# Kernel tuning notes

Measured on AMD Instinct MI355X. Metric: run time of the kernel, lower is better.

The kernel has to match this reference:

```python
import jax, jax.numpy as jnp
import numpy as np

SIZE = 2048
N_TASKS = 8
REDUCTION = 16
HID = SIZE // REDUCTION  # 128
B = 4096
INIT_STD = 0.01


def setup_inputs() -> dict:
    key = jax.random.key(0)
    k1, k2, k3 = jax.random.split(key, 3)
    x = jax.random.normal(k1, (B, SIZE), dtype=jnp.float32)
    task_id = jax.random.randint(k2, (B,), 0, N_TASKS, dtype=jnp.int64)
    kd, ku = jax.random.split(k3)
    # torch Linear weight is [out, in]; store transposed [in, out] per task
    Wd = jax.random.normal(kd, (N_TASKS, SIZE, HID), dtype=jnp.float32) * INIT_STD
    bd = jnp.zeros((N_TASKS, HID), dtype=jnp.float32)
    Wu = jax.random.normal(ku, (N_TASKS, HID, SIZE), dtype=jnp.float32) * INIT_STD
    bu = jnp.zeros((N_TASKS, SIZE), dtype=jnp.float32)
    return {"x": x, "Wd": Wd, "bd": bd, "Wu": Wu, "bu": bu, "task_id": task_id}


def reference(x, Wd, bd, Wu, bu, task_id):
    # residual=True (default). Compute every expert's adapter output densely
    # (T small), then combine per-sample by task_id; task_id == -1 -> passthrough.
    h = jax.nn.silu(jnp.einsum('bd,tdh->bth', x, Wd) + bd[None])        # [B,T,HID]
    out_all = jnp.einsum('bth,thd->btd', h, Wu) + bu[None]              # [B,T,SIZE]
    tid = jnp.clip(task_id, 0, N_TASKS - 1)
    out_sel = jnp.take_along_axis(out_all, tid[:, None, None], axis=1)[:, 0]  # [B,SIZE]
    valid = (task_id >= 0)[:, None]
    return jnp.where(valid, x + out_sel, x)
```

## Files before the change

### kernel.cpp

```cpp
#include <hip/hip_runtime.h>

#define BN 4096
#define SZ 2048
#define HIDN 128
#define NT 8
#define PADROWS 4384
#define PADTILES (PADROWS / 16)

typedef __bf16 bf16_t;
typedef bf16_t bf16x4 __attribute__((ext_vector_type(4)));
typedef bf16_t bf16x8 __attribute__((ext_vector_type(8)));
typedef float f32x4 __attribute__((ext_vector_type(4)));

__device__ inline bf16_t f2b(float f) {
    unsigned u = __builtin_bit_cast(unsigned, f);
    unsigned short s = (unsigned short)((u + 0x7fffu + ((u >> 16) & 1u)) >> 16);
    return __builtin_bit_cast(bf16_t, s);
}


__device__ inline int detect_i64(const int* task, int tid, int* sflag) {
    if (tid < 64) {
        int v = task[2 * tid + 1];
        bool ok = (v == 0 || v == -1);
        unsigned long long m = __ballot(ok);
        if (tid == 0) *sflag = (m == ~0ull) ? 1 : 0;
    }
    return 0;
}

__global__ __launch_bounds__(256) void k_prep(const float* __restrict__ Wd,
                                              const int* __restrict__ task,
                                              bf16_t* __restrict__ WdP,
                                              int* __restrict__ cnt16g) {
    int bid = blockIdx.x, tid = threadIdx.x;
    __shared__ int wv[4][9], sflag;
    if (bid >= 512) {
        int blk = bid - 512;
        int lane = tid & 63, w = tid >> 6;
        detect_i64(task, tid, &sflag);
        __syncthreads();
        int f = sflag;
        int item = blk * 256 + tid;
        int tv = f ? task[2 * item] : task[item];
        int bk = (tv < 0) ? 8 : (tv > 7 ? 7 : tv);
#pragma unroll
        for (int bu = 0; bu < 9; bu++) {
            unsigned long long m = __ballot(bk == bu);
            if (lane == 0) wv[w][bu] = (int)__popcll(m);
        }
        __syncthreads();
        if (tid < 9) {
            int s = 0;
#pragma unroll
            for (int ww = 0; ww < 4; ww++) s += wv[ww][tid];
            cnt16g[blk * 9 + tid] = s;
        }
        return;
    }
    __shared__ float tile[32][132];
    int t = bid >> 6, kt = bid & 63;
    const float* src = Wd + ((size_t)t * SZ + kt * 32) * HIDN;
    bf16_t* dst = WdP + ((size_t)(t * 8) * 64 + kt) * 512;
#pragma unroll
    for (int i = 0; i < 4; i++) {
        int row = (tid >> 5) + 8 * i, quad = tid & 31;
        f32x4 v = *(const f32x4*)(src + (size_t)row * HIDN + quad * 4);
        tile[row][quad * 4 + 0] = v.x; tile[row][quad * 4 + 1] = v.y;
        tile[row][quad * 4 + 2] = v.z; tile[row][quad * 4 + 3] = v.w;
    }
    __syncthreads();
    int w = tid >> 6, lane = tid & 63, lr = lane & 15, lq = lane >> 4;
#pragma unroll
    for (int ii = 0; ii < 2; ii++) {
        int hf = w * 2 + ii;
        bf16x8 o;
#pragma unroll
        for (int j = 0; j < 8; j++) {
            int kloc = (j < 4) ? (4 * lq + j) : (16 + 4 * lq + j - 4);
            o[j] = f2b(tile[kloc][hf * 16 + lr]);
        }
        *(bf16x8*)(dst + (size_t)hf * 64 * 512 + lane * 8) = o;
    }
}

__global__ __launch_bounds__(256) void k_scatter(const int* __restrict__ task,
                                                 const int* __restrict__ cnt16g,
                                                 int* __restrict__ meta,
                                                 int* __restrict__ idxb) {
    __shared__ int c16s[16][9], tot[9], pre9[9], off[10], wv[4][9], sflag;
    int tid = threadIdx.x, lane = tid & 63, w = tid >> 6, blk = blockIdx.x;
    detect_i64(task, tid, &sflag);
    if (tid < 144) ((int*)c16s)[tid] = cnt16g[tid];
    __syncthreads();
    int f = sflag;
    int item = blk * 256 + tid;
    int tv = f ? task[2 * item] : task[item];
    int bk = (tv < 0) ? 8 : (tv > 7 ? 7 : tv);
    unsigned long long mymask = 0;
#pragma unroll
    for (int bu = 0; bu < 9; bu++) {
        unsigned long long m = __ballot(bk == bu);
        if (lane == 0) wv[w][bu] = (int)__popcll(m);
        if (bk == bu) mymask = m;
    }
    int rank = (int)__popcll(mymask & ((1ull << lane) - 1ull));
    __syncthreads();
    if (tid < 9) {
        int t = 0;
#pragma unroll
        for (int b = 0; b < 16; b++) t += c16s[b][tid];
        tot[tid] = t;
        int p = 0;
        for (int b = 0; b < blk; b++) p += c16s[b][tid];
        pre9[tid] = p;
        int s = 0;
#pragma unroll
        for (int ww = 0; ww < 4; ww++) { int q = wv[ww][tid]; wv[ww][tid] = s; s += q; }
    }
    __syncthreads();
    if (tid == 0) {
        int s = 0;
        for (int i = 0; i < 9; i++) { off[i] = s; s += (tot[i] + 31) & ~31; }
        off[9] = s;
    }
    __syncthreads();
    int pos = off[bk] + pre9[bk] + wv[w][bk] + rank;
    idxb[pos] = item;
    if (blk == 0) {
        if (tid < 9) meta[tid] = tot[tid];
        if (tid >= 16 && tid < 26) meta[tid] = off[tid - 16];
    }
}

__global__ __launch_bounds__(256) void k_gemm1(const float* __restrict__ x,
                                               const float* __restrict__ Wu,
                                               const bf16_t* __restrict__ WdP,
                                               bf16_t* __restrict__ WuP,
                                               const float* __restrict__ bd,
                                               const int* __restrict__ idxb,
                                               const int* __restrict__ meta,
                                               bf16_t* __restrict__ HbP) {
    int bid = blockIdx.x;
    int tid = threadIdx.x, lane = tid & 63, w = tid >> 6;
    int lr = lane & 15, lq = lane >> 4;
    if (bid >= 4096) {
        __shared__ float tile[32][132];
        int lb = bid - 4096;
        int t = lb >> 6, rem = lb & 63;
        int kf = rem >> 4, cch = rem & 15;
        const float* src = Wu + ((size_t)t * HIDN + kf * 32) * SZ + cch * 128;
        bf16_t* dst = WuP + ((size_t)(t * 128 + cch * 8) * 4 + kf) * 512;
#pragma unroll
        for (int i = 0; i < 4; i++) {
            int row = (tid >> 5) + 8 * i, quad = tid & 31;
            f32x4 v = *(const f32x4*)(src + (size_t)row * SZ + quad * 4);
            tile[row][quad * 4 + 0] = v.x; tile[row][quad * 4 + 1] = v.y;
            tile[row][quad * 4 + 2] = v.z; tile[row][quad * 4 + 3] = v.w;
        }
        __syncthreads();
#pragma unroll
        for (int ii = 0; ii < 2; ii++) {
            int hf = w * 2 + ii;
            bf16x8 o;
#pragma unroll
            for (int j = 0; j < 8; j++) {
                int kloc = (j < 4) ? (4 * lq + j) : (16 + 4 * lq + j - 4);
                o[j] = f2b(tile[kloc][hf * 16 + lr]);
            }
            *(bf16x8*)(dst + (size_t)hf * 4 * 512 + lane * 8) = o;
        }
        return;
    }
    int t = bid & 7, hh = (bid >> 3) & 1, tile = bid >> 4;
    int n = meta[t];
    int r0 = tile * 16;
    if (r0 >= n) return;
    int base = meta[16 + t];

    __shared__ int sg[16];
    __shared__ bf16_t xl[2][16][260];
    __shared__ bf16_t hl[16][68];
    if (tid < 16) {
        int r = r0 + tid;
        sg[tid] = idxb[base + (r < n ? r : n - 1)];
    }
    __syncthreads();

    f32x4 pre[4];
#pragma unroll
    for (int rr = 0; rr < 4; rr++)
        pre[rr] = *(const f32x4*)(x + (size_t)sg[w * 4 + rr] * SZ + lane * 4);
#pragma unroll
    for (int rr = 0; rr < 4; rr++) {
        bf16x4 v = {f2b(pre[rr].x), f2b(pre[rr].y), f2b(pre[rr].z), f2b(pre[rr].w)};
        *(bf16x4*)(&xl[0][w * 4 + rr][lane * 4]) = v;
    }
    __syncthreads();

    const bf16_t* wb = WdP + ((size_t)(t * 8 + hh * 4 + w) * 64) * 512 + lane * 8;
    f32x4 acc = {};
    for (int c = 0; c < 8; c++) {
        int cur = c & 1;
        if (c < 7) {
#pragma unroll
            for (int rr = 0; rr < 4; rr++)
                pre[rr] = *(const f32x4*)(x + (size_t)sg[w * 4 + rr] * SZ +
                                          (c + 1) * 256 + lane * 4);
        }
#pragma unroll
        for (int k8 = 0; k8 < 8; k8++) {
            int kf = c * 8 + k8;
            bf16x4 alo = *(const bf16x4*)(&xl[cur][lr][k8 * 32 + 4 * lq]);
            bf16x4 ahi = *(const bf16x4*)(&xl[cur][lr][k8 * 32 + 16 + 4 * lq]);
            bf16x8 a;
            a[0] = alo[0]; a[1] = alo[1]; a[2] = alo[2]; a[3] = alo[3];
            a[4] = ahi[0]; a[5] = ahi[1]; a[6] = ahi[2]; a[7] = ahi[3];
            bf16x8 b = *(const bf16x8*)(wb + (size_t)kf * 512);
            acc = __builtin_amdgcn_mfma_f32_16x16x32_bf16(a, b, acc, 0, 0, 0);
        }
        if (c < 7) {
#pragma unroll
            for (int rr = 0; rr < 4; rr++) {
                bf16x4 v = {f2b(pre[rr].x), f2b(pre[rr].y), f2b(pre[rr].z), f2b(pre[rr].w)};
                *(bf16x4*)(&xl[cur ^ 1][w * 4 + rr][lane * 4]) = v;
            }
        }
        __syncthreads();
    }

    {
        float bb = bd[t * HIDN + hh * 64 + w * 16 + lr];
#pragma unroll
        for (int reg = 0; reg < 4; reg++) {
            float v = acc[reg] + bb;
            hl[4 * lq + reg][w * 16 + lr] = f2b(v / (1.f + __expf(-v)));
        }
    }
    __syncthreads();
    if (w < 2) {
        int rt = (base + r0) >> 4;
        bf16x8 o;
#pragma unroll
        for (int j = 0; j < 8; j++) {
            int k = w * 32 + ((j < 4) ? (4 * lq + j) : (16 + 4 * lq + j - 4));
            o[j] = hl[lr][k];
        }
        *(bf16x8*)(HbP + ((size_t)(rt * 4 + hh * 2 + w) * 64 + lane) * 8) = o;
    }
}

__global__ __launch_bounds__(256) void k_gemm2(const float* __restrict__ x,
                                               const bf16_t* __restrict__ WuP,
                                               const float* __restrict__ bu,
                                               const bf16_t* __restrict__ HbP,
                                               const int* __restrict__ idxb,
                                               const int* __restrict__ meta,
                                               float* __restrict__ out) {
    int bid = blockIdx.x;
    int tid = threadIdx.x;
    if (bid >= 16384) {
        int pb = bid - 16384;
        int n8 = meta[8];
        int tile = pb & 127, half = pb >> 7;
        int r0 = tile * 32;
        if (r0 >= n8) return;
        int base8 = meta[16 + 8];
        int row = tid >> 3, cq = tid & 7;
        int r = r0 + row;
        if (r < n8) {
            int g = idxb[base8 + r];
            const f32x4* xs = (const f32x4*)(x + (size_t)g * SZ + half * 256) + cq;
            f32x4* os = (f32x4*)(out + (size_t)g * SZ + half * 256) + cq;
#pragma unroll
            for (int j = 0; j < 8; j++) __builtin_nontemporal_store(xs[j * 8], &os[j * 8]);
        }
        return;
    }
    int t = bid & 7, tile = (bid >> 3) & 127, cchunk = bid >> 10;
    int n = meta[t];
    int r0 = tile * 32;
    if (r0 >= n) return;
    int base = meta[16 + t];
    int lane = tid & 63, w = tid >> 6;
    int wr = w & 1, wc = w >> 1, lr = lane & 15, lq = lane >> 4;

    int rt = (base + r0) / 16 + wr;
    const bf16_t* ap = HbP + (size_t)rt * 4 * 512 + lane * 8;
    bf16x8 a[4];
#pragma unroll
    for (int kf = 0; kf < 4; kf++) a[kf] = *(const bf16x8*)(ap + kf * 512);

    const bf16_t* bp = WuP + ((size_t)(t * 128 + cchunk * 8 + wc * 4) * 4) * 512 + lane * 8;
    f32x4 acc[4] = {};
#pragma unroll
    for (int cf = 0; cf < 4; cf++) {
#pragma unroll
        for (int kf = 0; kf < 4; kf++) {
            bf16x8 b = *(const bf16x8*)(bp + (size_t)(cf * 4 + kf) * 512);
            acc[cf] = __builtin_amdgcn_mfma_f32_16x16x32_bf16(a[kf], b, acc[cf], 0, 0, 0);
        }
    }

    int gr[4];
#pragma unroll
    for (int reg = 0; reg < 4; reg++) {
        int r = r0 + wr * 16 + 4 * lq + reg;
        gr[reg] = (r < n) ? idxb[base + r] : -1;
    }
#pragma unroll
    for (int cf = 0; cf < 4; cf++) {
        int c = cchunk * 128 + wc * 64 + cf * 16 + lr;
        float bb = bu[t * SZ + c];
#pragma unroll
        for (int reg = 0; reg < 4; reg++) {
            if (gr[reg] >= 0) {
                size_t o = (size_t)gr[reg] * SZ + c;
                __builtin_nontemporal_store(x[o] + acc[cf][reg] + bb, &out[o]);
            }
        }
    }
}

extern "C" void kernel_launch(void* const* d_in, const int* in_sizes, int n_in,
                              void* d_out, int out_size, void* d_ws, size_t ws_size,
                              hipStream_t stream) {
    const float* x  = (const float*)d_in[0];
    const float* Wd = (const float*)d_in[1];
    const float* bd = (const float*)d_in[2];
    const float* Wu = (const float*)d_in[3];
    const float* bu = (const float*)d_in[4];
    const int* task = (const int*)d_in[5];
    float* out = (float*)d_out;

    char* ws = (char*)d_ws;
    int* idxb    = (int*)ws;
    int* meta    = (int*)(ws + 17664);
    int* cnt16   = (int*)(ws + 17920);
    bf16_t* HbP  = (bf16_t*)(ws + 18560);
    bf16_t* WdP  = (bf16_t*)(ws + 1140864);
    bf16_t* WuP  = (bf16_t*)(ws + 5335168);

    k_prep<<<528, 256, 0, stream>>>(Wd, task, WdP, cnt16);
    k_scatter<<<16, 256, 0, stream>>>(task, cnt16, meta, idxb);
    k_gemm1<<<4096 + 512, 256, 0, stream>>>(x, Wu, WdP, WuP, bd, idxb, meta, HbP);
    k_gemm2<<<16384 + 1024, 256, 0, stream>>>(x, WuP, bu, HbP, idxb, meta, out);
}
```

Baseline: 48.73 us.

## Merge scatter into prep kernel and split MFMA accumulator chain

Drops the separate k_scatter launch. Each of the 16 bucketing blocks in k_prep now redundantly scans all 4096 task ids to compute the global per-bucket counts and prefix offsets itself, then writes its own items into idxb. This removes one kernel launch and the global count round-trip, at the cost of 16x redundant counting work and many block barriers. Separately, the gemm1 inner loop alternates between two accumulators so consecutive MFMAs are not serially dependent, and sums them at the end.

```diff
diff --git a/kernel.cpp b/kernel.cpp
--- a/kernel.cpp
+++ b/kernel.cpp
@@ -19,42 +19,66 @@
 }
 
 
-__device__ inline int detect_i64(const int* task, int tid, int* sflag) {
-    if (tid < 64) {
-        int v = task[2 * tid + 1];
-        bool ok = (v == 0 || v == -1);
-        unsigned long long m = __ballot(ok);
-        if (tid == 0) *sflag = (m == ~0ull) ? 1 : 0;
-    }
-    return 0;
-}
-
 __global__ __launch_bounds__(256) void k_prep(const float* __restrict__ Wd,
                                               const int* __restrict__ task,
                                               bf16_t* __restrict__ WdP,
-                                              int* __restrict__ cnt16g) {
+                                              int* __restrict__ meta,
+                                              int* __restrict__ idxb) {
     int bid = blockIdx.x, tid = threadIdx.x;
-    __shared__ int wv[4][9], sflag;
     if (bid >= 512) {
+        __shared__ int c16s[16][9], tot[9], pre9[9], off[10], wv[4][9], sflag;
         int blk = bid - 512;
         int lane = tid & 63, w = tid >> 6;
-        detect_i64(task, tid, &sflag);
+        if (tid < 64) {
+            int v = task[2 * tid + 1];
+            bool ok = (v == 0 || v == -1);
+            unsigned long long m = __ballot(ok);
+            if (tid == 0) sflag = (m == ~0ull) ? 1 : 0;
+        }
         __syncthreads();
         int f = sflag;
-        int item = blk * 256 + tid;
-        int tv = f ? task[2 * item] : task[item];
-        int bk = (tv < 0) ? 8 : (tv > 7 ? 7 : tv);
-#pragma unroll
-        for (int bu = 0; bu < 9; bu++) {
-            unsigned long long m = __ballot(bk == bu);
-            if (lane == 0) wv[w][bu] = (int)__popcll(m);
-        }
-        __syncthreads();
+        int mybk = 0, myrank = 0, myprew = 0;
+        for (int s = 0; s < 16; s++) {
+            int item = s * 256 + tid;
+            int tv = f ? task[2 * item] : task[item];
+            int bk = (tv < 0) ? 8 : (tv > 7 ? 7 : tv);
+            unsigned long long mymask = 0;
+#pragma unroll
+            for (int bu = 0; bu < 9; bu++) {
+                unsigned long long m = __ballot(bk == bu);
+                if (lane == 0) wv[w][bu] = (int)__popcll(m);
+                if (bk == bu) mymask = m;
+            }
+            __syncthreads();
+            if (s == blk) {
+                mybk = bk;
+                myrank = (int)__popcll(mymask & ((1ull << lane) - 1ull));
+                myprew = 0;
+                for (int ww = 0; ww < w; ww++) myprew += wv[ww][bk];
+            }
+            if (tid < 9) c16s[s][tid] = wv[0][tid] + wv[1][tid] + wv[2][tid] + wv[3][tid];
+            __syncthreads();
+        }
         if (tid < 9) {
+            int t = 0;
+#pragma unroll
+            for (int s = 0; s < 16; s++) t += c16s[s][tid];
+            tot[tid] = t;
+            int p = 0;
+            for (int s = 0; s < blk; s++) p += c16s[s][tid];
+            pre9[tid] = p;
+        }
+        __syncthreads();
+        if (tid == 0) {
             int s = 0;
-#pragma unroll
-            for (int ww = 0; ww < 4; ww++) s += wv[ww][tid];
-            cnt16g[blk * 9 + tid] = s;
+            for (int i = 0; i < 9; i++) { off[i] = s; s += (tot[i] + 31) & ~31; }
+            off[9] = s;
+        }
+        __syncthreads();
+        idxb[off[mybk] + pre9[mybk] + myprew + myrank] = blk * 256 + tid;
+        if (blk == 0) {
+            if (tid < 9) meta[tid] = tot[tid];
+            if (tid >= 16 && tid < 26) meta[tid] = off[tid - 16];
         }
         return;
     }
@@ -81,55 +105,6 @@
             o[j] = f2b(tile[kloc][hf * 16 + lr]);
         }
         *(bf16x8*)(dst + (size_t)hf * 64 * 512 + lane * 8) = o;
-    }
-}
-
-__global__ __launch_bounds__(256) void k_scatter(const int* __restrict__ task,
-                                                 const int* __restrict__ cnt16g,
-                                                 int* __restrict__ meta,
-                                                 int* __restrict__ idxb) {
-    __shared__ int c16s[16][9], tot[9], pre9[9], off[10], wv[4][9], sflag;
-    int tid = threadIdx.x, lane = tid & 63, w = tid >> 6, blk = blockIdx.x;
-    detect_i64(task, tid, &sflag);
-    if (tid < 144) ((int*)c16s)[tid] = cnt16g[tid];
-    __syncthreads();
-    int f = sflag;
-    int item = blk * 256 + tid;
-    int tv = f ? task[2 * item] : task[item];
-    int bk = (tv < 0) ? 8 : (tv > 7 ? 7 : tv);
-    unsigned long long mymask = 0;
-#pragma unroll
-    for (int bu = 0; bu < 9; bu++) {
-        unsigned long long m = __ballot(bk == bu);
-        if (lane == 0) wv[w][bu] = (int)__popcll(m);
-        if (bk == bu) mymask = m;
-    }
-    int rank = (int)__popcll(mymask & ((1ull << lane) - 1ull));
-    __syncthreads();
-    if (tid < 9) {
-        int t = 0;
-#pragma unroll
-        for (int b = 0; b < 16; b++) t += c16s[b][tid];
-        tot[tid] = t;
-        int p = 0;
-        for (int b = 0; b < blk; b++) p += c16s[b][tid];
-        pre9[tid] = p;
-        int s = 0;
-#pragma unroll
-        for (int ww = 0; ww < 4; ww++) { int q = wv[ww][tid]; wv[ww][tid] = s; s += q; }
-    }
-    __syncthreads();
-    if (tid == 0) {
-        int s = 0;
-        for (int i = 0; i < 9; i++) { off[i] = s; s += (tot[i] + 31) & ~31; }
-        off[9] = s;
-    }
-    __syncthreads();
-    int pos = off[bk] + pre9[bk] + wv[w][bk] + rank;
-    idxb[pos] = item;
-    if (blk == 0) {
-        if (tid < 9) meta[tid] = tot[tid];
-        if (tid >= 16 && tid < 26) meta[tid] = off[tid - 16];
     }
 }
 
@@ -199,7 +174,7 @@
     __syncthreads();
 
     const bf16_t* wb = WdP + ((size_t)(t * 8 + hh * 4 + w) * 64) * 512 + lane * 8;
-    f32x4 acc = {};
+    f32x4 acc0 = {}, acc1 = {};
     for (int c = 0; c < 8; c++) {
         int cur = c & 1;
         if (c < 7) {
@@ -217,7 +192,10 @@
             a[0] = alo[0]; a[1] = alo[1]; a[2] = alo[2]; a[3] = alo[3];
             a[4] = ahi[0]; a[5] = ahi[1]; a[6] = ahi[2]; a[7] = ahi[3];
             bf16x8 b = *(const bf16x8*)(wb + (size_t)kf * 512);
-            acc = __builtin_amdgcn_mfma_f32_16x16x32_bf16(a, b, acc, 0, 0, 0);
+            if (k8 & 1)
+                acc1 = __builtin_amdgcn_mfma_f32_16x16x32_bf16(a, b, acc1, 0, 0, 0);
+            else
+                acc0 = __builtin_amdgcn_mfma_f32_16x16x32_bf16(a, b, acc0, 0, 0, 0);
         }
         if (c < 7) {
 #pragma unroll
@@ -228,6 +206,7 @@
         }
         __syncthreads();
     }
+    f32x4 acc = acc0 + acc1;
 
     {
         float bb = bd[t * HIDN + hh * 64 + w * 16 + lr];
@@ -336,13 +315,11 @@
     char* ws = (char*)d_ws;
     int* idxb    = (int*)ws;
     int* meta    = (int*)(ws + 17664);
-    int* cnt16   = (int*)(ws + 17920);
     bf16_t* HbP  = (bf16_t*)(ws + 18560);
     bf16_t* WdP  = (bf16_t*)(ws + 1140864);
     bf16_t* WuP  = (bf16_t*)(ws + 5335168);
 
-    k_prep<<<528, 256, 0, stream>>>(Wd, task, WdP, cnt16);
-    k_scatter<<<16, 256, 0, stream>>>(task, cnt16, meta, idxb);
+    k_prep<<<528, 256, 0, stream>>>(Wd, task, WdP, meta, idxb);
     k_gemm1<<<4096 + 512, 256, 0, stream>>>(x, Wu, WdP, WuP, bd, idxb, meta, HbP);
     k_gemm2<<<16384 + 1024, 256, 0, stream>>>(x, WuP, bu, HbP, idxb, meta, out);
 }
```

New measurement: 54.23 us. 11.3% more time.

## Split gemm1 K dimension across two wave groups with LDS reduction

Applied to the files above, without the earlier changes.

Doubles k_gemm1 block size to 512 threads. In the GEMM path, two groups of four waves each handle half of the 2048-wide K range, and their partial accumulators are summed through shared memory before bias and SiLU. The Wu repack path now processes two tiles per block, halving its block count. The goal is to shorten the serial K loop per block and raise the number of waves in flight. The cost is larger shared memory per block, an extra reduction step with barriers, and possibly lower block occupancy.

```diff
diff --git a/kernel.cpp b/kernel.cpp
--- a/kernel.cpp
+++ b/kernel.cpp
@@ -133,7 +133,7 @@
     }
 }
 
-__global__ __launch_bounds__(256) void k_gemm1(const float* __restrict__ x,
+__global__ __launch_bounds__(512) void k_gemm1(const float* __restrict__ x,
                                                const float* __restrict__ Wu,
                                                const bf16_t* __restrict__ WdP,
                                                bf16_t* __restrict__ WuP,
@@ -141,34 +141,36 @@
                                                const int* __restrict__ idxb,
                                                const int* __restrict__ meta,
                                                bf16_t* __restrict__ HbP) {
+    __shared__ __align__(16) char smem[40192];
     int bid = blockIdx.x;
-    int tid = threadIdx.x, lane = tid & 63, w = tid >> 6;
-    int lr = lane & 15, lq = lane >> 4;
+    int tid = threadIdx.x;
     if (bid >= 4096) {
-        __shared__ float tile[32][132];
-        int lb = bid - 4096;
+        float (*tile2)[32][132] = (float (*)[32][132])smem;
+        int half = tid >> 8, t256 = tid & 255;
+        int lb = (bid - 4096) * 2 + half;
         int t = lb >> 6, rem = lb & 63;
         int kf = rem >> 4, cch = rem & 15;
         const float* src = Wu + ((size_t)t * HIDN + kf * 32) * SZ + cch * 128;
         bf16_t* dst = WuP + ((size_t)(t * 128 + cch * 8) * 4 + kf) * 512;
 #pragma unroll
         for (int i = 0; i < 4; i++) {
-            int row = (tid >> 5) + 8 * i, quad = tid & 31;
+            int row = (t256 >> 5) + 8 * i, quad = t256 & 31;
             f32x4 v = *(const f32x4*)(src + (size_t)row * SZ + quad * 4);
-            tile[row][quad * 4 + 0] = v.x; tile[row][quad * 4 + 1] = v.y;
-            tile[row][quad * 4 + 2] = v.z; tile[row][quad * 4 + 3] = v.w;
+            tile2[half][row][quad * 4 + 0] = v.x; tile2[half][row][quad * 4 + 1] = v.y;
+            tile2[half][row][quad * 4 + 2] = v.z; tile2[half][row][quad * 4 + 3] = v.w;
         }
         __syncthreads();
+        int w2 = t256 >> 6, lane2 = t256 & 63, lr2 = lane2 & 15, lq2 = lane2 >> 4;
 #pragma unroll
         for (int ii = 0; ii < 2; ii++) {
-            int hf = w * 2 + ii;
+            int hf2 = w2 * 2 + ii;
             bf16x8 o;
 #pragma unroll
             for (int j = 0; j < 8; j++) {
-                int kloc = (j < 4) ? (4 * lq + j) : (16 + 4 * lq + j - 4);
-                o[j] = f2b(tile[kloc][hf * 16 + lr]);
+                int kloc = (j < 4) ? (4 * lq2 + j) : (16 + 4 * lq2 + j - 4);
+                o[j] = f2b(tile2[half][kloc][hf2 * 16 + lr2]);
             }
-            *(bf16x8*)(dst + (size_t)hf * 4 * 512 + lane * 8) = o;
+            *(bf16x8*)(dst + (size_t)hf2 * 4 * 512 + lane2 * 8) = o;
         }
         return;
     }
@@ -177,10 +179,15 @@
     int r0 = tile * 16;
     if (r0 >= n) return;
     int base = meta[16 + t];
-
-    __shared__ int sg[16];
-    __shared__ bf16_t xl[2][16][260];
-    __shared__ bf16_t hl[16][68];
+    int lane = tid & 63, w16 = tid >> 6;
+    int hf = w16 & 3, kg = w16 >> 2;
+    int lr = lane & 15, lq = lane >> 4;
+
+    int* sg = (int*)smem;
+    bf16_t (*xl)[2][16][260] = (bf16_t (*)[2][16][260])(smem + 64);
+    bf16_t (*hl)[68] = (bf16_t (*)[68])(smem + 33344);
+    float (*red)[68] = (float (*)[68])(smem + 35520);
+
     if (tid < 16) {
         int r = r0 + tid;
         sg[tid] = idxb[base + (r < n ? r : n - 1)];
@@ -190,63 +197,69 @@
     f32x4 pre[4];
 #pragma unroll
     for (int rr = 0; rr < 4; rr++)
-        pre[rr] = *(const f32x4*)(x + (size_t)sg[w * 4 + rr] * SZ + lane * 4);
+        pre[rr] = *(const f32x4*)(x + (size_t)sg[hf * 4 + rr] * SZ + kg * 1024 + lane * 4);
 #pragma unroll
     for (int rr = 0; rr < 4; rr++) {
         bf16x4 v = {f2b(pre[rr].x), f2b(pre[rr].y), f2b(pre[rr].z), f2b(pre[rr].w)};
-        *(bf16x4*)(&xl[0][w * 4 + rr][lane * 4]) = v;
-    }
-    __syncthreads();
-
-    const bf16_t* wb = WdP + ((size_t)(t * 8 + hh * 4 + w) * 64) * 512 + lane * 8;
+        *(bf16x4*)(&xl[kg][0][hf * 4 + rr][lane * 4]) = v;
+    }
+    __syncthreads();
+
+    const bf16_t* wb = WdP + ((size_t)(t * 8 + hh * 4 + hf) * 64) * 512 + lane * 8;
     f32x4 acc = {};
-    for (int c = 0; c < 8; c++) {
+    for (int c = 0; c < 4; c++) {
         int cur = c & 1;
-        if (c < 7) {
+        if (c < 3) {
 #pragma unroll
             for (int rr = 0; rr < 4; rr++)
-                pre[rr] = *(const f32x4*)(x + (size_t)sg[w * 4 + rr] * SZ +
-                                          (c + 1) * 256 + lane * 4);
+                pre[rr] = *(const f32x4*)(x + (size_t)sg[hf * 4 + rr] * SZ +
+                                          kg * 1024 + (c + 1) * 256 + lane * 4);
         }
 #pragma unroll
         for (int k8 = 0; k8 < 8; k8++) {
-            int kf = c * 8 + k8;
-            bf16x4 alo = *(const bf16x4*)(&xl[cur][lr][k8 * 32 + 4 * lq]);
-            bf16x4 ahi = *(const bf16x4*)(&xl[cur][lr][k8 * 32 + 16 + 4 * lq]);
+            int kf = kg * 32 + c * 8 + k8;
+            bf16x4 alo = *(const bf16x4*)(&xl[kg][cur][lr][k8 * 32 + 4 * lq]);
+            bf16x4 ahi = *(const bf16x4*)(&xl[kg][cur][lr][k8 * 32 + 16 + 4 * lq]);
             bf16x8 a;
             a[0] = alo[0]; a[1] = alo[1]; a[2] = alo[2]; a[3] = alo[3];
             a[4] = ahi[0]; a[5] = ahi[1]; a[6] = ahi[2]; a[7] = ahi[3];
             bf16x8 b = *(const bf16x8*)(wb + (size_t)kf * 512);
             acc = __builtin_amdgcn_mfma_f32_16x16x32_bf16(a, b, acc, 0, 0, 0);
         }
-        if (c < 7) {
+        if (c < 3) {
 #pragma unroll
             for (int rr = 0; rr < 4; rr++) {
                 bf16x4 v = {f2b(pre[rr].x), f2b(pre[rr].y), f2b(pre[rr].z), f2b(pre[rr].w)};
-                *(bf16x4*)(&xl[cur ^ 1][w * 4 + rr][lane * 4]) = v;
+                *(bf16x4*)(&xl[kg][cur ^ 1][hf * 4 + rr][lane * 4]) = v;
             }
         }
         __syncthreads();
     }
 
-    {
-        float bb = bd[t * HIDN + hh * 64 + w * 16 + lr];
+    if (kg == 1) {
+#pragma unroll
+        for (int reg = 0; reg < 4; reg++)
+            red[4 * lq + reg][hf * 16 + lr] = acc[reg];
+    }
+    __syncthreads();
+    if (kg == 0) {
+        float bb = bd[t * HIDN + hh * 64 + hf * 16 + lr];
 #pragma unroll
         for (int reg = 0; reg < 4; reg++) {
-            float v = acc[reg] + bb;
-            hl[4 * lq + reg][w * 16 + lr] = f2b(v / (1.f + __expf(-v)));
-        }
-    }
-    __syncthreads();
-    if (w < 2) {
+            float v = acc[reg] + red[4 * lq + reg][hf * 16 + lr] + bb;
+            hl[4 * lq + reg][hf * 16 + lr] = f2b(v / (1.f + __expf(-v)));
+        }
+    }
+    __syncthreads();
+    if (kg == 0 && hf < 2) {
         int rt = (base + r0) >> 4;
         bf16x8 o;
 #pragma unroll
         for (int j = 0; j < 8; j++) {
-            int k = w * 32 + ((j < 4) ? (4 * lq + j) : (16 + 4 * lq + j - 4));
+            int k = hf * 32 + ((j < 4) ? (4 * lq + j) : (16 + 4 * lq + j - 4));
             o[j] = hl[lr][k];
         }
-        *(bf16x8*)(HbP + ((size_t)(rt * 4 + hh * 2 + w) * 64 + lane) * 8) = o;
+        *(bf16x8*)(HbP + ((size_t)(rt * 4 + hh * 2 + hf) * 64 + lane) * 8) = o;
     }
 }
 
@@ -343,6 +356,6 @@
 
     k_prep<<<528, 256, 0, stream>>>(Wd, task, WdP, cnt16);
     k_scatter<<<16, 256, 0, stream>>>(task, cnt16, meta, idxb);
-    k_gemm1<<<4096 + 512, 256, 0, stream>>>(x, Wu, WdP, WuP, bd, idxb, meta, HbP);
+    k_gemm1<<<4096 + 256, 512, 0, stream>>>(x, Wu, WdP, WuP, bd, idxb, meta, HbP);
     k_gemm2<<<16384 + 1024, 256, 0, stream>>>(x, WuP, bu, HbP, idxb, meta, out);
 }
```

Measured after the change: 48.28 us (median of 2 runs). Within noise of the previous version (-0.9%).

## Map blocks to padded row tiles instead of per-task worst-case grids

Applied to the files above, without the earlier changes.

Both GEMM kernels now index blocks by global padded row tile and find the owning task by scanning the offset table, instead of launching a worst-case grid per task in which most blocks exit early. The gemm1 grid shrinks from 4096+512 blocks to 548+512, and gemm2 from 17408 to PADT32*16. The passthrough copy is folded into the same tile mapping. This removes the cost of launching and retiring thousands of empty blocks, at the price of a small per-block scan over the offsets.

```diff
diff --git a/kernel.cpp b/kernel.cpp
--- a/kernel.cpp
+++ b/kernel.cpp
@@ -6,6 +6,7 @@
 #define NT 8
 #define PADROWS 4384
 #define PADTILES (PADROWS / 16)
+#define PADT32 (PADROWS / 32)
 
 typedef __bf16 bf16_t;
 typedef bf16_t bf16x4 __attribute__((ext_vector_type(4)));
@@ -144,9 +145,10 @@
     int bid = blockIdx.x;
     int tid = threadIdx.x, lane = tid & 63, w = tid >> 6;
     int lr = lane & 15, lq = lane >> 4;
-    if (bid >= 4096) {
+    if (bid >= 548) {
+        int lb = bid - 548;
+        if (lb >= 512) return;
         __shared__ float tile[32][132];
-        int lb = bid - 4096;
         int t = lb >> 6, rem = lb & 63;
         int kf = rem >> 4, cch = rem & 15;
         const float* src = Wu + ((size_t)t * HIDN + kf * 32) * SZ + cch * 128;
@@ -172,11 +174,19 @@
         }
         return;
     }
-    int t = bid & 7, hh = (bid >> 3) & 1, tile = bid >> 4;
-    int n = meta[t];
-    int r0 = tile * 16;
+    int rt = bid >> 1, hh = bid & 1;
+    int row0 = rt * 16;
+    int off[10];
+#pragma unroll
+    for (int i = 0; i < 10; i++) off[i] = meta[16 + i];
+    int t = 8;
+#pragma unroll
+    for (int b = 0; b < 8; b++)
+        if (row0 >= off[b] && row0 < off[b + 1]) t = b;
+    if (t == 8) return;
+    int base = off[t], n = meta[t];
+    int r0 = row0 - base;
     if (r0 >= n) return;
-    int base = meta[16 + t];
 
     __shared__ int sg[16];
     __shared__ bf16_t xl[2][16][260];
@@ -239,7 +249,6 @@
     }
     __syncthreads();
     if (w < 2) {
-        int rt = (base + r0) >> 4;
         bf16x8 o;
 #pragma unroll
         for (int j = 0; j < 8; j++) {
@@ -259,29 +268,34 @@
                                                float* __restrict__ out) {
     int bid = blockIdx.x;
     int tid = threadIdx.x;
-    if (bid >= 16384) {
-        int pb = bid - 16384;
-        int n8 = meta[8];
-        int tile = pb & 127, half = pb >> 7;
-        int r0 = tile * 32;
-        if (r0 >= n8) return;
-        int base8 = meta[16 + 8];
+    int rt32 = bid >> 4, cchunk = bid & 15;
+    int row0 = rt32 * 32;
+    int off[10];
+#pragma unroll
+    for (int i = 0; i < 10; i++) off[i] = meta[16 + i];
+    int t = -1;
+#pragma unroll
+    for (int b = 0; b < 9; b++)
+        if (row0 >= off[b] && row0 < off[b + 1]) t = b;
+    if (t < 0) return;
+    int base = off[t], n = meta[t];
+    int r0 = row0 - base;
+    if (r0 >= n) return;
+
+    if (t == 8) {
         int row = tid >> 3, cq = tid & 7;
         int r = r0 + row;
-        if (r < n8) {
-            int g = idxb[base8 + r];
-            const f32x4* xs = (const f32x4*)(x + (size_t)g * SZ + half * 256) + cq;
-            f32x4* os = (f32x4*)(out + (size_t)g * SZ + half * 256) + cq;
-#pragma unroll
-            for (int j = 0; j < 8; j++) __builtin_nontemporal_store(xs[j * 8], &os[j * 8]);
+        if (r < n) {
+            int g = idxb[base + r];
+            const f32x4* xs = (const f32x4*)(x + (size_t)g * SZ + cchunk * 128);
+            f32x4* os = (f32x4*)(out + (size_t)g * SZ + cchunk * 128);
+#pragma unroll
+            for (int j = 0; j < 4; j++)
+                __builtin_nontemporal_store(xs[cq + j * 8], &os[cq + j * 8]);
         }
         return;
     }
-    int t = bid & 7, tile = (bid >> 3) & 127, cchunk = bid >> 10;
-    int n = meta[t];
-    int r0 = tile * 32;
-    if (r0 >= n) return;
-    int base = meta[16 + t];
+
     int lane = tid & 63, w = tid >> 6;
     int wr = w & 1, wc = w >> 1, lr = lane & 15, lq = lane >> 4;
 
@@ -343,6 +357,6 @@
 
     k_prep<<<528, 256, 0, stream>>>(Wd, task, WdP, cnt16);
     k_scatter<<<16, 256, 0, stream>>>(task, cnt16, meta, idxb);
-    k_gemm1<<<4096 + 512, 256, 0, stream>>>(x, Wu, WdP, WuP, bd, idxb, meta, HbP);
-    k_gemm2<<<16384 + 1024, 256, 0, stream>>>(x, WuP, bu, HbP, idxb, meta, out);
-}
+    k_gemm1<<<548 + 512, 256, 0, stream>>>(x, Wu, WdP, WuP, bd, idxb, meta, HbP);
+    k_gemm2<<<PADT32 * 16, 256, 0, stream>>>(x, WuP, bu, HbP, idxb, meta, out);
+}
```

Result: slower. 54.03 us (+10.9%).
